# Performance work log

Hardware: AMD Instinct MI355X
Metric: run time of the kernel (lower is better)

## Reference

```python
import jax, jax.numpy as jnp
import numpy as np

V, H, L, S, B = 32000, 1024, 4, 256, 16


def setup_inputs() -> dict:
    key = jax.random.key(0)
    ks = jax.random.split(key, 6)
    s = 0.02  # init scale
    return {
        "x": jax.random.randint(ks[0], (S, B), 0, V, dtype=jnp.int32),
        "h0": jnp.zeros((L, B, H), jnp.float32),
        "c0": jnp.zeros((L, B, H), jnp.float32),
        "emb": jax.random.normal(ks[1], (V, H), jnp.float32) * s,
        "W_ih": jax.random.normal(ks[2], (L, 4 * H, H), jnp.float32) * s,
        "W_hh": jax.random.normal(ks[3], (L, 4 * H, H), jnp.float32) * s,
        "b_ih": jnp.zeros((L, 4 * H), jnp.float32),
        "b_hh": jnp.zeros((L, 4 * H), jnp.float32),
        "fc_W": jax.random.normal(ks[4], (V, H), jnp.float32) * s,
        "fc_b": jnp.zeros((V,), jnp.float32),
    }


def _lstm_layer(xs, h0, c0, Wih, Whh, b):
    # xs: [S, B, Hin]; torch gate order is (i, f, g, o)
    def step(carry, x_t):
        h, c = carry
        z = x_t @ Wih.T + h @ Whh.T + b  # [B, 4H]
        i, f, g, o = jnp.split(z, 4, axis=-1)
        c = jax.nn.sigmoid(f) * c + jax.nn.sigmoid(i) * jnp.tanh(g)
        h = jax.nn.sigmoid(o) * jnp.tanh(c)
        return (h, c), h

    (hT, cT), ys = jax.lax.scan(step, (h0, c0), xs)
    return ys, hT, cT


def reference(x, h0, c0, emb, W_ih, W_hh, b_ih, b_hh, fc_W, fc_b):
    y = emb[x]  # [S, B, H]
    h_fin, c_fin = [], []
    for l in range(L):  # fixed small layer count; time dim handled by scan
        y, hT, cT = _lstm_layer(y, h0[l], c0[l], W_ih[l], W_hh[l], b_ih[l] + b_hh[l])
        h_fin.append(hT)
        c_fin.append(cT)
    logits = y @ fc_W.T + fc_b  # [S, B, V]
    return logits, jnp.stack(h_fin), jnp.stack(c_fin)
```

## Files before the change

kernel.cpp:

```cpp
#include <hip/hip_runtime.h>
#include <hip/hip_bf16.h>

typedef unsigned short u16;
typedef short short8 __attribute__((ext_vector_type(8)));
typedef u16 u16x8 __attribute__((ext_vector_type(8)));
typedef float f32x4 __attribute__((ext_vector_type(4)));

#define H 1024
#define NB 16
#define SEQ 256
#define NL 4
#define VOCAB 32000
#define G4 4096
#define YSZ ((size_t)SEQ * NB * H)

__device__ __forceinline__ u16 f2bf(float f) {
  __hip_bfloat16 h = __float2bfloat16(f);
  return *reinterpret_cast<u16*>(&h);
}
__device__ __forceinline__ float sigm(float x) { return 1.0f / (1.0f + __expf(-x)); }
__device__ __forceinline__ float tanhfast(float x) { return 2.0f / (1.0f + __expf(-2.0f * x)) - 1.0f; }

__device__ __forceinline__ f32x4 mfma16(short8 a, short8 b, f32x4 c) {
  return __builtin_amdgcn_mfma_f32_16x16x32_bf16(a, b, c, 0, 0, 0);
}

template <int BOFF>
__device__ __forceinline__ short8 ldg_sc(const u16* p) {
  short8 r;
  asm volatile("global_load_dwordx4 %0, %1, off offset:%2 sc0 sc1"
               : "=&v"(r) : "v"(p), "n"(BOFF));
  return r;
}

#define WAITV0                                                 \
  do {                                                         \
    asm volatile("s_waitcnt vmcnt(0)" ::: "memory");           \
    __builtin_amdgcn_sched_barrier(0);                         \
  } while (0)

#define LD8SC(d, p)                                            \
  do {                                                         \
    d[0] = ldg_sc<0 * 64>(p); d[1] = ldg_sc<1 * 64>(p);        \
    d[2] = ldg_sc<2 * 64>(p); d[3] = ldg_sc<3 * 64>(p);        \
    d[4] = ldg_sc<4 * 64>(p); d[5] = ldg_sc<5 * 64>(p);        \
    d[6] = ldg_sc<6 * 64>(p); d[7] = ldg_sc<7 * 64>(p);        \
  } while (0)


__global__ void cvt_bf16(const float* __restrict__ in, u16* __restrict__ out, int n8) {
  const int i = blockIdx.x * blockDim.x + threadIdx.x;
  if (i >= n8) return;
  const float4 a = ((const float4*)in)[2 * i];
  const float4 b = ((const float4*)in)[2 * i + 1];
  u16x8 o;
  o[0] = f2bf(a.x); o[1] = f2bf(a.y); o[2] = f2bf(a.z); o[3] = f2bf(a.w);
  o[4] = f2bf(b.x); o[5] = f2bf(b.y); o[6] = f2bf(b.z); o[7] = f2bf(b.w);
  *(u16x8*)(out + (size_t)i * 8) = o;
}

__global__ void bias_sum(const float* __restrict__ a, const float* __restrict__ b,
                         float* __restrict__ o, int n) {
  const int i = blockIdx.x * blockDim.x + threadIdx.x;
  if (i < n) o[i] = a[i] + b[i];
}

__global__ void zero_u32(unsigned* __restrict__ p, int n) {
  const int i = blockIdx.x * blockDim.x + threadIdx.x;
  if (i < n) p[i] = 0u;
}

__global__ void gather_emb(const int* __restrict__ x, const float* __restrict__ emb,
                           u16* __restrict__ Y) {
  const int row = blockIdx.x;
  const int tok = x[row];
  const float4 v = ((const float4*)(emb + (size_t)tok * H))[threadIdx.x];
  ushort4 o;
  o.x = f2bf(v.x); o.y = f2bf(v.y); o.z = f2bf(v.z); o.w = f2bf(v.w);
  *(ushort4*)(Y + (size_t)row * H + threadIdx.x * 4) = o;
}

__device__ __forceinline__ void wavewait(const unsigned* __restrict__ base, unsigned tgt) {
  const unsigned* p = base + (threadIdx.x & 63) * 16;
  unsigned v;
  do {
    asm volatile("global_load_dword %0, %1, off sc0 sc1\n\ts_waitcnt vmcnt(0)"
                 : "=&v"(v) : "v"(p) : "memory");
  } while (!__all(v >= tgt));
  __builtin_amdgcn_sched_barrier(0);
}


__global__ __launch_bounds__(256, 1) void lstm_scan(
    const u16* __restrict__ ybase_r, u16* __restrict__ ybase_w,
    const u16* __restrict__ Wih_all, const u16* __restrict__ Whh_all,
    const float* __restrict__ bias_all, const u16* __restrict__ h0_all,
    const float* __restrict__ c0_all, float* __restrict__ hfin_all,
    float* __restrict__ cfin_all, unsigned* __restrict__ bars)
{
  extern __shared__ u16 sm[];
  u16* __restrict__ smw = sm;
  f32x4* __restrict__ lred = (f32x4*)(sm + 65536);
  u16* __restrict__ smh = sm + 73728;

  const int tid = threadIdx.x;
  const int lane = tid & 63;
  const int wid = tid >> 6;
  const int l = blockIdx.x >> 6;
  const int jgrp = blockIdx.x & 63;
  const int jbase = jgrp * 16;
  const int b = lane & 15;
  const int lg = lane >> 4;
  const int m = lane & 15;
  const int j = jbase + wid * 4 + lg;

  const u16* __restrict__ Yin  = ybase_r + (size_t)l * YSZ;
  u16* __restrict__ Yout       = ybase_w + (size_t)(l + 1) * YSZ;
  const u16* __restrict__ Wih  = Wih_all + (size_t)l * G4 * H;
  const u16* __restrict__ Whh  = Whh_all + (size_t)l * G4 * H;
  const float* __restrict__ bias = bias_all + (size_t)l * G4;
  const u16* __restrict__ h0b  = h0_all + (size_t)l * NB * H;
  const float* __restrict__ c0 = c0_all + (size_t)l * NB * H;
  float* __restrict__ hfin     = hfin_all + (size_t)l * NB * H;
  float* __restrict__ cfin     = cfin_all + (size_t)l * NB * H;
  unsigned* __restrict__ myflags = bars + l * 1024;
  const unsigned* __restrict__ xflags = bars + (l - 1) * 1024;
  unsigned* __restrict__ myflag_wr = myflags + jgrp * 16;

  #pragma unroll
  for (int rt = 0; rt < 4; ++rt) {
    const size_t ar = (size_t)((m & 3) * H + jbase + rt * 4 + (m >> 2));
    const u16* src = Whh + ar * H + lg * 8;
    #pragma unroll
    for (int i = 0; i < 8; ++i) {
      const int ks = wid * 8 + i;
      short8 w = *(const short8*)(src + ks * 32);
      *(short8*)(smw + (size_t)rt * 16384 + (size_t)ks * 512 + lane * 8) = w;
    }
  }
  short8 WI[32];
  #pragma unroll
  for (int rt = 0; rt < 4; ++rt) {
    const size_t ar = (size_t)((m & 3) * H + jbase + rt * 4 + (m >> 2));
    const u16* src = Wih + ar * H + lg * 8;
    #pragma unroll
    for (int i = 0; i < 8; ++i) {
      WI[rt * 8 + i] = *(const short8*)(src + (wid * 8 + i) * 32);
      asm volatile("" : "+v"(WI[rt * 8 + i]));
    }
  }
  __syncthreads();

  f32x4 bias4;
  bias4[0] = bias[0 * H + j];
  bias4[1] = bias[1 * H + j];
  bias4[2] = bias[2 * H + j];
  bias4[3] = bias[3 * H + j];

  float c = c0[b * H + j];
  const int boff = b * H + lg * 8;
  const int kboff = wid * 256;
  const u16* __restrict__ smwv = smw + (size_t)wid * 4096 + lane * 8;

  for (int t = 0; t < SEQ; ++t) {
    const u16* xw = Yin + (size_t)t * (NB * H) + boff + kboff;

    f32x4 a0 = {0.f, 0.f, 0.f, 0.f};
    f32x4 a1 = {0.f, 0.f, 0.f, 0.f};
    f32x4 a2 = {0.f, 0.f, 0.f, 0.f};
    f32x4 a3 = {0.f, 0.f, 0.f, 0.f};

    short8 fx[8];
    if (l == 0) {
      #pragma unroll
      for (int i = 0; i < 8; ++i) fx[i] = *(const short8*)(xw + i * 32);
    } else {
      wavewait(xflags, (unsigned)(t + 1));
      LD8SC(fx, xw);
      WAITV0;
    }
    #pragma unroll
    for (int i = 0; i < 8; ++i) {
      a0 = mfma16(WI[0 * 8 + i], fx[i], a0);
      a1 = mfma16(WI[1 * 8 + i], fx[i], a1);
      a2 = mfma16(WI[2 * 8 + i], fx[i], a2);
      a3 = mfma16(WI[3 * 8 + i], fx[i], a3);
    }

    short8 fh[8];
    if (t == 0) {
      const u16* hw = h0b + boff + kboff;
      #pragma unroll
      for (int i = 0; i < 8; ++i) fh[i] = *(const short8*)(hw + i * 32);
    } else {
      const u16* hw = Yout + (size_t)(t - 1) * (NB * H) + boff + kboff;
      wavewait(myflags, (unsigned)t);
      LD8SC(fh, hw);
      WAITV0;
    }
    #pragma unroll
    for (int i = 0; i < 8; ++i) {
      short8 w0 = *(const short8*)(smwv + 0 * 16384 + i * 512);
      short8 w1 = *(const short8*)(smwv + 1 * 16384 + i * 512);
      short8 w2 = *(const short8*)(smwv + 2 * 16384 + i * 512);
      short8 w3 = *(const short8*)(smwv + 3 * 16384 + i * 512);
      a0 = mfma16(w0, fh[i], a0);
      a1 = mfma16(w1, fh[i], a1);
      a2 = mfma16(w2, fh[i], a2);
      a3 = mfma16(w3, fh[i], a3);
    }

    if (wid != 0) lred[(0 * 4 + wid) * 64 + lane] = a0;
    if (wid != 1) lred[(1 * 4 + wid) * 64 + lane] = a1;
    if (wid != 2) lred[(2 * 4 + wid) * 64 + lane] = a2;
    if (wid != 3) lred[(3 * 4 + wid) * 64 + lane] = a3;
    __syncthreads();

    f32x4 z4 = bias4;
    if (wid == 0)      z4 += a0;
    else if (wid == 1) z4 += a1;
    else if (wid == 2) z4 += a2;
    else               z4 += a3;
    #pragma unroll
    for (int w2 = 0; w2 < 4; ++w2)
      if (w2 != wid) z4 += lred[(wid * 4 + w2) * 64 + lane];

    const float ig = sigm(z4[0]);
    const float fg = sigm(z4[1]);
    const float gg = tanhfast(z4[2]);
    const float og = sigm(z4[3]);
    c = fg * c + ig * gg;
    const float h = og * tanhfast(c);

    smh[b * 16 + wid * 4 + lg] = f2bf(h);
    if (t == SEQ - 1) {
      hfin[b * H + j] = h;
      cfin[b * H + j] = c;
    }

    __syncthreads();
    if (wid == 0) {
      if (lane < 32) {
        const int br = lane >> 1, half = lane & 1;
        u16x8 pv = *(const u16x8*)&smh[br * 16 + half * 8];
        const u16* dst = Yout + (size_t)t * (NB * H) + (size_t)br * H + jbase + half * 8;
        asm volatile("global_store_dwordx4 %0, %1, off sc0 sc1"
                     :: "v"(dst), "v"(pv) : "memory");
      }
      asm volatile("s_waitcnt vmcnt(0)" ::: "memory");
      if (lane == 0) {
        const unsigned tv = (unsigned)(t + 1);
        asm volatile("global_store_dword %0, %1, off sc0 sc1"
                     :: "v"(myflag_wr), "v"(tv) : "memory");
      }
    }
  }
}


__global__ __launch_bounds__(256, 1) void gemm_bt_bias(
    const u16* __restrict__ A, const u16* __restrict__ Bw,
    const float* __restrict__ bias, float* __restrict__ C, int N)
{
  __shared__ u16 As[128 * 64];
  __shared__ u16 Bs[128 * 64];
  const int tid = threadIdx.x;
  const int lane = tid & 63;
  const int wid = tid >> 6;
  const int m0 = blockIdx.x * 128;
  const int n0 = blockIdx.y * 128;
  const int wr = wid >> 1, wc = wid & 1;
  const int lr = lane >> 3;
  const int lc = (lane & 7) * 8;
  f32x4 acc[4][4] = {};

  for (int k0 = 0; k0 < H; k0 += 64) {
    __syncthreads();
    #pragma unroll
    for (int cc = 0; cc < 4; ++cc) {
      const int row = wid * 32 + cc * 8 + lr;
      __builtin_amdgcn_global_load_lds(
          (const __attribute__((address_space(1))) void*)(A + (size_t)(m0 + row) * H + k0 + lc),
          (__attribute__((address_space(3))) void*)(As + row * 64 + lc), 16, 0, 0);
      __builtin_amdgcn_global_load_lds(
          (const __attribute__((address_space(1))) void*)(Bw + (size_t)(n0 + row) * H + k0 + lc),
          (__attribute__((address_space(3))) void*)(Bs + row * 64 + lc), 16, 0, 0);
    }
    __syncthreads();
    #pragma unroll
    for (int ks = 0; ks < 2; ++ks) {
      short8 af[4], bfr[4];
      #pragma unroll
      for (int i = 0; i < 4; ++i) {
        af[i]  = *(const short8*)&As[(wr * 64 + i * 16 + (lane & 15)) * 64 + ks * 32 + (lane >> 4) * 8];
        bfr[i] = *(const short8*)&Bs[(wc * 64 + i * 16 + (lane & 15)) * 64 + ks * 32 + (lane >> 4) * 8];
      }
      #pragma unroll
      for (int i = 0; i < 4; ++i) {
        #pragma unroll
        for (int jj = 0; jj < 4; ++jj)
          acc[i][jj] = mfma16(af[i], bfr[jj], acc[i][jj]);
      }
    }
  }

  #pragma unroll
  for (int jj = 0; jj < 4; ++jj) {
    const int col = n0 + wc * 64 + jj * 16 + (lane & 15);
    const float bv = bias[col];
    #pragma unroll
    for (int i = 0; i < 4; ++i) {
      const int rbase = m0 + wr * 64 + i * 16 + (lane >> 4) * 4;
      #pragma unroll
      for (int r = 0; r < 4; ++r)
        C[(size_t)(rbase + r) * N + col] = acc[i][jj][r] + bv;
    }
  }
}


extern "C" void kernel_launch(void* const* d_in, const int* in_sizes, int n_in,
                              void* d_out, int out_size, void* d_ws, size_t ws_size,
                              hipStream_t stream) {
  const int*   x    = (const int*)d_in[0];
  const float* h0   = (const float*)d_in[1];
  const float* c0   = (const float*)d_in[2];
  const float* emb  = (const float*)d_in[3];
  const float* W_ih = (const float*)d_in[4];
  const float* W_hh = (const float*)d_in[5];
  const float* b_ih = (const float*)d_in[6];
  const float* b_hh = (const float*)d_in[7];
  const float* fc_W = (const float*)d_in[8];
  const float* fc_b = (const float*)d_in[9];
  float* out = (float*)d_out;
  char* ws = (char*)d_ws;

  size_t off = 0;
  u16* WihB = (u16*)(ws + off); off += (size_t)NL * G4 * H * 2;
  u16* WhhB = (u16*)(ws + off); off += (size_t)NL * G4 * H * 2;
  u16* fcWB = (u16*)(ws + off); off += (size_t)VOCAB * H * 2;
  u16* h0B  = (u16*)(ws + off); off += (size_t)NL * NB * H * 2;
  float* biasB = (float*)(ws + off); off += (size_t)NL * G4 * 4;
  u16* ybufs = (u16*)(ws + off); off += (size_t)(NL + 1) * YSZ * 2;
  unsigned* bars = (unsigned*)(ws + off); off += 16384;
  if (ws_size < off) return;

  int n8;
  n8 = NL * G4 * H / 8;  cvt_bf16<<<(n8 + 255) / 256, 256, 0, stream>>>(W_ih, WihB, n8);
  n8 = NL * G4 * H / 8;  cvt_bf16<<<(n8 + 255) / 256, 256, 0, stream>>>(W_hh, WhhB, n8);
  n8 = VOCAB * H / 8;    cvt_bf16<<<(n8 + 255) / 256, 256, 0, stream>>>(fc_W, fcWB, n8);
  n8 = NL * NB * H / 8;  cvt_bf16<<<(n8 + 255) / 256, 256, 0, stream>>>(h0, h0B, n8);
  bias_sum<<<(NL * G4 + 255) / 256, 256, 0, stream>>>(b_ih, b_hh, biasB, NL * G4);
  zero_u32<<<16, 256, 0, stream>>>(bars, 4096);
  gather_emb<<<SEQ * NB, 256, 0, stream>>>(x, emb, ybufs);

  float* hfin = out + (size_t)SEQ * NB * VOCAB;
  float* cfin = hfin + (size_t)NL * NB * H;

  lstm_scan<<<NL * 64, 256, 147968, stream>>>(
      ybufs, ybufs, WihB, WhhB, biasB, h0B, c0, hfin, cfin, bars);

  gemm_bt_bias<<<dim3(32, 250), 256, 0, stream>>>(
      ybufs + (size_t)NL * YSZ, fcWB, fc_b, out, VOCAB);
}
```

Before: 1.709 ms.

## Stream W_ih from global per step and widen FC GEMM tile to 128x256

The LSTM scan stops holding the input-weight fragments in registers and instead reloads them from global memory (via cache) at every timestep. This frees registers but adds load latency to each step of the serial recurrence. Separately, the output projection GEMM moves from 128x128 to 128x256 tiles with 8 accumulators per row-tile, which doubles per-wave accumulator state and halves the grid, aiming for more reuse of A. The xflags pointer is also clamped so that layer 0 does not form an out-of-range address.

Result: slower. 3.465 ms (+102.8%).

```diff
diff --git a/kernel.cpp b/kernel.cpp
--- a/kernel.cpp
+++ b/kernel.cpp
@@ -124,7 +124,7 @@
   float* __restrict__ hfin     = hfin_all + (size_t)l * NB * H;
   float* __restrict__ cfin     = cfin_all + (size_t)l * NB * H;
   unsigned* __restrict__ myflags = bars + l * 1024;
-  const unsigned* __restrict__ xflags = bars + (l - 1) * 1024;
+  const unsigned* __restrict__ xflags = bars + (l > 0 ? (l - 1) : 0) * 1024;
   unsigned* __restrict__ myflag_wr = myflags + jgrp * 16;
 
   #pragma unroll
@@ -138,17 +138,10 @@
       *(short8*)(smw + (size_t)rt * 16384 + (size_t)ks * 512 + lane * 8) = w;
     }
   }
-  short8 WI[32];
-  #pragma unroll
-  for (int rt = 0; rt < 4; ++rt) {
-    const size_t ar = (size_t)((m & 3) * H + jbase + rt * 4 + (m >> 2));
-    const u16* src = Wih + ar * H + lg * 8;
-    #pragma unroll
-    for (int i = 0; i < 8; ++i) {
-      WI[rt * 8 + i] = *(const short8*)(src + (wid * 8 + i) * 32);
-      asm volatile("" : "+v"(WI[rt * 8 + i]));
-    }
-  }
+  const u16* __restrict__ wr0 = Wih + (size_t)((m & 3) * H + jbase + 0 * 4 + (m >> 2)) * H + (wid * 8) * 32 + lg * 8;
+  const u16* __restrict__ wr1 = Wih + (size_t)((m & 3) * H + jbase + 1 * 4 + (m >> 2)) * H + (wid * 8) * 32 + lg * 8;
+  const u16* __restrict__ wr2 = Wih + (size_t)((m & 3) * H + jbase + 2 * 4 + (m >> 2)) * H + (wid * 8) * 32 + lg * 8;
+  const u16* __restrict__ wr3 = Wih + (size_t)((m & 3) * H + jbase + 3 * 4 + (m >> 2)) * H + (wid * 8) * 32 + lg * 8;
   __syncthreads();
 
   f32x4 bias4;
@@ -181,10 +174,10 @@
     }
     #pragma unroll
     for (int i = 0; i < 8; ++i) {
-      a0 = mfma16(WI[0 * 8 + i], fx[i], a0);
-      a1 = mfma16(WI[1 * 8 + i], fx[i], a1);
-      a2 = mfma16(WI[2 * 8 + i], fx[i], a2);
-      a3 = mfma16(WI[3 * 8 + i], fx[i], a3);
+      a0 = mfma16(*(const short8*)(wr0 + i * 32), fx[i], a0);
+      a1 = mfma16(*(const short8*)(wr1 + i * 32), fx[i], a1);
+      a2 = mfma16(*(const short8*)(wr2 + i * 32), fx[i], a2);
+      a3 = mfma16(*(const short8*)(wr3 + i * 32), fx[i], a3);
     }
 
     short8 fh[8];
@@ -263,16 +256,17 @@
     const float* __restrict__ bias, float* __restrict__ C, int N)
 {
   __shared__ u16 As[128 * 64];
-  __shared__ u16 Bs[128 * 64];
+  __shared__ u16 Bs[256 * 64];
   const int tid = threadIdx.x;
   const int lane = tid & 63;
   const int wid = tid >> 6;
   const int m0 = blockIdx.x * 128;
-  const int n0 = blockIdx.y * 128;
-  const int wr = wid >> 1, wc = wid & 1;
+  const int n0 = blockIdx.y * 256;
+  const int wr = wid >> 1;
+  const int wc = wid & 1;
   const int lr = lane >> 3;
   const int lc = (lane & 7) * 8;
-  f32x4 acc[4][4] = {};
+  f32x4 acc[4][8] = {};
 
   for (int k0 = 0; k0 < H; k0 += 64) {
     __syncthreads();
@@ -282,6 +276,10 @@
       __builtin_amdgcn_global_load_lds(
           (const __attribute__((address_space(1))) void*)(A + (size_t)(m0 + row) * H + k0 + lc),
           (__attribute__((address_space(3))) void*)(As + row * 64 + lc), 16, 0, 0);
+    }
+    #pragma unroll
+    for (int cc = 0; cc < 8; ++cc) {
+      const int row = wid * 64 + cc * 8 + lr;
       __builtin_amdgcn_global_load_lds(
           (const __attribute__((address_space(1))) void*)(Bw + (size_t)(n0 + row) * H + k0 + lc),
           (__attribute__((address_space(3))) void*)(Bs + row * 64 + lc), 16, 0, 0);
@@ -289,24 +287,25 @@
     __syncthreads();
     #pragma unroll
     for (int ks = 0; ks < 2; ++ks) {
-      short8 af[4], bfr[4];
-      #pragma unroll
-      for (int i = 0; i < 4; ++i) {
+      short8 af[4], bfr[8];
+      #pragma unroll
+      for (int i = 0; i < 4; ++i)
         af[i]  = *(const short8*)&As[(wr * 64 + i * 16 + (lane & 15)) * 64 + ks * 32 + (lane >> 4) * 8];
-        bfr[i] = *(const short8*)&Bs[(wc * 64 + i * 16 + (lane & 15)) * 64 + ks * 32 + (lane >> 4) * 8];
-      }
+      #pragma unroll
+      for (int jj = 0; jj < 8; ++jj)
+        bfr[jj] = *(const short8*)&Bs[(wc * 128 + jj * 16 + (lane & 15)) * 64 + ks * 32 + (lane >> 4) * 8];
       #pragma unroll
       for (int i = 0; i < 4; ++i) {
         #pragma unroll
-        for (int jj = 0; jj < 4; ++jj)
+        for (int jj = 0; jj < 8; ++jj)
           acc[i][jj] = mfma16(af[i], bfr[jj], acc[i][jj]);
       }
     }
   }
 
   #pragma unroll
-  for (int jj = 0; jj < 4; ++jj) {
-    const int col = n0 + wc * 64 + jj * 16 + (lane & 15);
+  for (int jj = 0; jj < 8; ++jj) {
+    const int col = n0 + wc * 128 + jj * 16 + (lane & 15);
     const float bv = bias[col];
     #pragma unroll
     for (int i = 0; i < 4; ++i) {
@@ -360,6 +359,6 @@
   lstm_scan<<<NL * 64, 256, 147968, stream>>>(
       ybufs, ybufs, WihB, WhhB, biasB, h0B, c0, hfin, cfin, bars);
 
-  gemm_bt_bias<<<dim3(32, 250), 256, 0, stream>>>(
+  gemm_bt_bias<<<dim3(32, 125), 256, 0, stream>>>(
       ybufs + (size_t)NL * YSZ, fcWB, fc_b, out, VOCAB);
 }
```
